# Kernel tuning notes

Measured on AMD Instinct MI355X. Metric: run time of the kernel, lower is better.

The kernel has to match this reference:

```python
import jax, jax.numpy as jnp
import numpy as np

N_NODES = 100000
N_EDGES = 600000
D_FEAT = 128
EDIM = 128
N_CLASSES = 10


def setup_inputs() -> dict:
    key = jax.random.key(0)
    k_h, k_eh, k_w, k_b, k_s, k_d = jax.random.split(key, 6)
    h = jax.random.normal(k_h, (N_NODES, D_FEAT), dtype=jnp.float32)
    edge_h = jax.random.normal(k_eh, (N_EDGES, 1, EDIM), dtype=jnp.float32)
    # Linear(in_features*2 + edim -> out_classes); torch stores weight as [out, in]
    W_w = jax.random.normal(k_w, (N_CLASSES, 2 * D_FEAT + EDIM), dtype=jnp.float32) * 0.05
    W_b = jax.random.normal(k_b, (N_CLASSES,), dtype=jnp.float32) * 0.05
    src = jax.random.randint(k_s, (N_EDGES,), 0, N_NODES, dtype=jnp.int64)
    dst = jax.random.randint(k_d, (N_EDGES,), 0, N_NODES, dtype=jnp.int64)
    return {"h": h, "edge_h": edge_h, "W_w": W_w, "W_b": W_b, "src": src, "dst": dst}


def reference(h, edge_h, W_w, W_b, src, dst):
    # edge-wise gather of src/dst node features
    h_u = h[src]                      # [E, D]
    h_v = h[dst]                      # [E, D]
    h_uv = edge_h.reshape(edge_h.shape[0], edge_h.shape[2])  # [E, edim]
    feat = jnp.concatenate([h_u, h_v, h_uv], axis=1)          # [E, 2D+edim]
    score = feat @ W_w.T + W_b                                 # [E, C]
    return score
```

## Files before the change

### kernel.cpp

```cpp
#include <hip/hip_runtime.h>


typedef __attribute__((ext_vector_type(8))) short short8;
typedef __attribute__((ext_vector_type(4))) float f32x4;

#define NC   10
#define TPW  4
#define NFRAG 12

__device__ __forceinline__ unsigned short f2bf(float f) {
    unsigned u = __builtin_bit_cast(unsigned, f);
    u += 0x7FFFu + ((u >> 16) & 1u);
    return (unsigned short)(u >> 16);
}

__device__ __forceinline__ short8 cvt8(f32x4 a, f32x4 b) {
    short8 s;
    s[0]=(short)f2bf(a[0]); s[1]=(short)f2bf(a[1]);
    s[2]=(short)f2bf(a[2]); s[3]=(short)f2bf(a[3]);
    s[4]=(short)f2bf(b[0]); s[5]=(short)f2bf(b[1]);
    s[6]=(short)f2bf(b[2]); s[7]=(short)f2bf(b[3]);
    return s;
}

__global__ void build_wfrag(const float* __restrict__ Ww, short8* __restrict__ frag) {
    const int l = threadIdx.x;
    const int n = l & 15;
    const int q = l >> 4;
#pragma unroll
    for (int t = 0; t < NFRAG; ++t) {
        short8 b = (short8)0;
        if (n < NC) {
            const float* w = Ww + n * 384 + t * 32 + q * 8;
            const f32x4 w0 = *(const f32x4*)(w);
            const f32x4 w1 = *(const f32x4*)(w + 4);
            b = cvt8(w0, w1);
        }
        frag[t * 64 + l] = b;
    }
}

#define LG(v0,v1,v2,v3,v4,v5,v6,v7,p)           \
    v0 = *(const f32x4*)((p) + 0);              \
    v1 = *(const f32x4*)((p) + 4);              \
    v2 = *(const f32x4*)((p) + 32);             \
    v3 = *(const f32x4*)((p) + 36);             \
    v4 = *(const f32x4*)((p) + 64);             \
    v5 = *(const f32x4*)((p) + 68);             \
    v6 = *(const f32x4*)((p) + 96);             \
    v7 = *(const f32x4*)((p) + 100);

#define CG(g, v0,v1,v2,v3,v4,v5,v6,v7)                                        \
    acc = __builtin_amdgcn_mfma_f32_16x16x32_bf16(cvt8(v0,v1), bf[(g)*4+0], acc, 0,0,0); \
    acc = __builtin_amdgcn_mfma_f32_16x16x32_bf16(cvt8(v2,v3), bf[(g)*4+1], acc, 0,0,0); \
    acc = __builtin_amdgcn_mfma_f32_16x16x32_bf16(cvt8(v4,v5), bf[(g)*4+2], acc, 0,0,0); \
    acc = __builtin_amdgcn_mfma_f32_16x16x32_bf16(cvt8(v6,v7), bf[(g)*4+3], acc, 0,0,0);

__global__ __launch_bounds__(64, 3) void mlp_edge_mfma(
    const float* __restrict__ h,
    const float* __restrict__ eh,
    const short8* __restrict__ frag,
    const float* __restrict__ Wb,
    const int*   __restrict__ src,
    const int*   __restrict__ dst,
    float* __restrict__ out,
    int E)
{
    const int l = threadIdx.x;
    const int n = l & 15;
    const int q = l >> 4;

    short8 bf[NFRAG];
#pragma unroll
    for (int t = 0; t < NFRAG; ++t) bf[t] = frag[t * 64 + l];
    const float bias = (n < NC) ? Wb[n] : 0.f;

    const long tile0 = (long)blockIdx.x * TPW;

#pragma unroll 1
    for (int tt = 0; tt < TPW; ++tt) {
        const long base = (tile0 + tt) * 16;
        if (base >= E) break;
        const long e  = base + n;
        const long ec = (e < E) ? e : (long)(E - 1);
        const float* ps = h  + (long)src[ec] * 128 + q * 8;
        const float* pd = h  + (long)dst[ec] * 128 + q * 8;
        const float* pe = eh + ec * 128 + q * 8;

        f32x4 x0,x1,x2,x3,x4,x5,x6,x7;
        f32x4 y0,y1,y2,y3,y4,y5,y6,y7;

        f32x4 acc = {0.f, 0.f, 0.f, 0.f};

        LG(x0,x1,x2,x3,x4,x5,x6,x7, ps)
        LG(y0,y1,y2,y3,y4,y5,y6,y7, pd)
        CG(0, x0,x1,x2,x3,x4,x5,x6,x7)
        LG(x0,x1,x2,x3,x4,x5,x6,x7, pe)
        CG(1, y0,y1,y2,y3,y4,y5,y6,y7)
        CG(2, x0,x1,x2,x3,x4,x5,x6,x7)

        if (n < NC) {
#pragma unroll
            for (int r = 0; r < 4; ++r) {
                const long e2 = base + q * 4 + r;
                if (e2 < E) out[e2 * NC + n] = acc[r] + bias;
            }
        }
    }
}

extern "C" void kernel_launch(void* const* d_in, const int* in_sizes, int n_in,
                              void* d_out, int out_size, void* d_ws, size_t ws_size,
                              hipStream_t stream) {
    const float* h   = (const float*)d_in[0];
    const float* eh  = (const float*)d_in[1];
    const float* Ww  = (const float*)d_in[2];
    const float* Wb  = (const float*)d_in[3];
    const int*   src = (const int*)d_in[4];
    const int*   dst = (const int*)d_in[5];
    float* out = (float*)d_out;

    const int E = in_sizes[4];
    short8* frag = (short8*)d_ws;

    build_wfrag<<<1, 64, 0, stream>>>(Ww, frag);

    const int edgesPerBlock = 16 * TPW;
    const int blocks = (E + edgesPerBlock - 1) / edgesPerBlock;
    mlp_edge_mfma<<<blocks, 64, 0, stream>>>(h, eh, frag, Wb, src, dst, out, E);
}
```

Before: 495.3 us.

## Stream gathered rows into LDS via async global_load_lds with triple buffering

```diff
diff --git a/kernel.cpp b/kernel.cpp
--- a/kernel.cpp
+++ b/kernel.cpp
@@ -4,9 +4,11 @@
 typedef __attribute__((ext_vector_type(8))) short short8;
 typedef __attribute__((ext_vector_type(4))) float f32x4;
 
-#define NC   10
-#define TPW  4
+#define NC    10
+#define TPW   8
 #define NFRAG 12
+
+#define WAITVM(N) __builtin_amdgcn_s_waitcnt(((N)&0xF) | (7u<<4) | (0xFu<<8) | (((unsigned)(N)>>4)<<14))
 
 __device__ __forceinline__ unsigned short f2bf(float f) {
     unsigned u = __builtin_bit_cast(unsigned, f);
@@ -23,6 +25,13 @@
     return s;
 }
 
+__device__ __forceinline__ void dma16(const void* g, void* l) {
+    __builtin_amdgcn_global_load_lds(
+        (const __attribute__((address_space(1))) void*)g,
+        (__attribute__((address_space(3))) void*)l,
+        16, 0, 0);
+}
+
 __global__ void build_wfrag(const float* __restrict__ Ww, short8* __restrict__ frag) {
     const int l = threadIdx.x;
     const int n = l & 15;
@@ -32,31 +41,13 @@
         short8 b = (short8)0;
         if (n < NC) {
             const float* w = Ww + n * 384 + t * 32 + q * 8;
-            const f32x4 w0 = *(const f32x4*)(w);
-            const f32x4 w1 = *(const f32x4*)(w + 4);
-            b = cvt8(w0, w1);
+            b = cvt8(*(const f32x4*)w, *(const f32x4*)(w + 4));
         }
         frag[t * 64 + l] = b;
     }
 }
 
-#define LG(v0,v1,v2,v3,v4,v5,v6,v7,p)           \
-    v0 = *(const f32x4*)((p) + 0);              \
-    v1 = *(const f32x4*)((p) + 4);              \
-    v2 = *(const f32x4*)((p) + 32);             \
-    v3 = *(const f32x4*)((p) + 36);             \
-    v4 = *(const f32x4*)((p) + 64);             \
-    v5 = *(const f32x4*)((p) + 68);             \
-    v6 = *(const f32x4*)((p) + 96);             \
-    v7 = *(const f32x4*)((p) + 100);
-
-#define CG(g, v0,v1,v2,v3,v4,v5,v6,v7)                                        \
-    acc = __builtin_amdgcn_mfma_f32_16x16x32_bf16(cvt8(v0,v1), bf[(g)*4+0], acc, 0,0,0); \
-    acc = __builtin_amdgcn_mfma_f32_16x16x32_bf16(cvt8(v2,v3), bf[(g)*4+1], acc, 0,0,0); \
-    acc = __builtin_amdgcn_mfma_f32_16x16x32_bf16(cvt8(v4,v5), bf[(g)*4+2], acc, 0,0,0); \
-    acc = __builtin_amdgcn_mfma_f32_16x16x32_bf16(cvt8(v6,v7), bf[(g)*4+3], acc, 0,0,0);
-
-__global__ __launch_bounds__(64, 3) void mlp_edge_mfma(
+__global__ __launch_bounds__(64, 2) void mlp_edge_dma(
     const float* __restrict__ h,
     const float* __restrict__ eh,
     const short8* __restrict__ frag,
@@ -66,44 +57,87 @@
     float* __restrict__ out,
     int E)
 {
+    __shared__ __align__(16) char buf[3][8192];
+
     const int l = threadIdx.x;
     const int n = l & 15;
     const int q = l >> 4;
+
+    const long wbase = (long)blockIdx.x * (16 * TPW);
 
     short8 bf[NFRAG];
 #pragma unroll
     for (int t = 0; t < NFRAG; ++t) bf[t] = frag[t * 64 + l];
     const float bias = (n < NC) ? Wb[n] : 0.f;
 
-    const long tile0 = (long)blockIdx.x * TPW;
+    int sidx[TPW], didx[TPW], erow[TPW];
+#pragma unroll
+    for (int t = 0; t < TPW; ++t) {
+        const long er  = wbase + t * 16 + n;
+        const long erc = (er < E) ? er : (long)(E - 1);
+        sidx[t] = src[erc];
+        didx[t] = dst[erc];
+        erow[t] = (int)erc;
+    }
 
-#pragma unroll 1
-    for (int tt = 0; tt < TPW; ++tt) {
-        const long base = (tile0 + tt) * 16;
-        if (base >= E) break;
-        const long e  = base + n;
-        const long ec = (e < E) ? e : (long)(E - 1);
-        const float* ps = h  + (long)src[ec] * 128 + q * 8;
-        const float* pd = h  + (long)dst[ec] * 128 + q * 8;
-        const float* pe = eh + ec * 128 + q * 8;
+    f32x4 acc[TPW];
+#pragma unroll
+    for (int t = 0; t < TPW; ++t) acc[t] = (f32x4){0.f, 0.f, 0.f, 0.f};
 
-        f32x4 x0,x1,x2,x3,x4,x5,x6,x7;
-        f32x4 y0,y1,y2,y3,y4,y5,y6,y7;
+    const unsigned wb16 = (unsigned)q * 16u;
 
-        f32x4 acc = {0.f, 0.f, 0.f, 0.f};
+#define ISSUE_G(t, s) do {                                                    \
+    const char* gb;                                                           \
+    unsigned off;                                                             \
+    if ((s) == 0)      { gb = (const char*)h;  off = (unsigned)sidx[t] * 512u + wb16; } \
+    else if ((s) == 1) { gb = (const char*)h;  off = (unsigned)didx[t] * 512u + wb16; } \
+    else               { gb = (const char*)eh; off = (unsigned)erow[t] * 512u + wb16; } \
+    const char* ga = gb + off;                                                \
+    char* lb = &buf[(s)][0];                                                  \
+    _Pragma("unroll")                                                         \
+    for (int i = 0; i < 8; ++i) dma16(ga + i * 64, lb + i * 1024);            \
+} while (0)
 
-        LG(x0,x1,x2,x3,x4,x5,x6,x7, ps)
-        LG(y0,y1,y2,y3,y4,y5,y6,y7, pd)
-        CG(0, x0,x1,x2,x3,x4,x5,x6,x7)
-        LG(x0,x1,x2,x3,x4,x5,x6,x7, pe)
-        CG(1, y0,y1,y2,y3,y4,y5,y6,y7)
-        CG(2, x0,x1,x2,x3,x4,x5,x6,x7)
+#define CONSUME_G(t, s) do {                                                  \
+    const char* lb = &buf[(s)][0];                                            \
+    _Pragma("unroll")                                                         \
+    for (int t4 = 0; t4 < 4; ++t4) {                                          \
+        const int ib = (2 * t4 + (q >> 1)) * 1024 + ((q & 1) * 2) * 256 + n * 16; \
+        const f32x4 a0 = *(const f32x4*)(lb + ib);                            \
+        const f32x4 a1 = *(const f32x4*)(lb + ib + 256);                      \
+        acc[t] = __builtin_amdgcn_mfma_f32_16x16x32_bf16(                     \
+            cvt8(a0, a1), bf[(s) * 4 + t4], acc[t], 0, 0, 0);                 \
+    }                                                                         \
+} while (0)
 
-        if (n < NC) {
+    WAITVM(0);
+    __asm__ volatile("" ::: "memory");
+
+    ISSUE_G(0, 0); ISSUE_G(0, 1); ISSUE_G(0, 2);
+
+#pragma unroll
+    for (int t = 0; t < TPW; ++t) {
+#pragma unroll
+        for (int s = 0; s < 3; ++s) {
+            if (t < TPW - 1 || s == 0) { WAITVM(16); }
+            else if (s == 1)           { WAITVM(8);  }
+            else                       { WAITVM(0);  }
+            __asm__ volatile("" ::: "memory");
+            CONSUME_G(t, s);
+            if (t < TPW - 1) ISSUE_G(t + 1, s);
+        }
+    }
+#undef ISSUE_G
+#undef CONSUME_G
+
+    if (n < NC) {
+#pragma unroll
+        for (int t = 0; t < TPW; ++t) {
+            const long tb = wbase + t * 16;
 #pragma unroll
             for (int r = 0; r < 4; ++r) {
-                const long e2 = base + q * 4 + r;
-                if (e2 < E) out[e2 * NC + n] = acc[r] + bias;
+                const long e2 = tb + q * 4 + r;
+                if (e2 < E) out[e2 * NC + n] = acc[t][r] + bias;
             }
         }
     }
@@ -127,5 +161,5 @@
 
     const int edgesPerBlock = 16 * TPW;
     const int blocks = (E + edgesPerBlock - 1) / edgesPerBlock;
-    mlp_edge_mfma<<<blocks, 64, 0, stream>>>(h, eh, frag, Wb, src, dst, out, E);
+    mlp_edge_dma<<<blocks, 64, 0, stream>>>(h, eh, frag, Wb, src, dst, out, E);
 }
```

Result: no change. 490.8 us (-0.9%).

## Pre-convert node features to bf16 in workspace to halve gather traffic

Applied to the files above, without the earlier changes.

```diff
diff --git a/kernel.cpp b/kernel.cpp
--- a/kernel.cpp
+++ b/kernel.cpp
@@ -4,9 +4,10 @@
 typedef __attribute__((ext_vector_type(8))) short short8;
 typedef __attribute__((ext_vector_type(4))) float f32x4;
 
-#define NC   10
-#define TPW  4
+#define NC    10
+#define TPW   4
 #define NFRAG 12
+#define FRAG_BYTES 12288
 
 __device__ __forceinline__ unsigned short f2bf(float f) {
     unsigned u = __builtin_bit_cast(unsigned, f);
@@ -32,15 +33,23 @@
         short8 b = (short8)0;
         if (n < NC) {
             const float* w = Ww + n * 384 + t * 32 + q * 8;
-            const f32x4 w0 = *(const f32x4*)(w);
-            const f32x4 w1 = *(const f32x4*)(w + 4);
-            b = cvt8(w0, w1);
+            b = cvt8(*(const f32x4*)w, *(const f32x4*)(w + 4));
         }
         frag[t * 64 + l] = b;
     }
 }
 
-#define LG(v0,v1,v2,v3,v4,v5,v6,v7,p)           \
+__global__ __launch_bounds__(256) void cvt_h_kernel(
+    const float* __restrict__ h, short8* __restrict__ hb, long n8) {
+    const long i = (long)blockIdx.x * 256 + threadIdx.x;
+    if (i < n8) {
+        const f32x4 a = *(const f32x4*)(h + i * 8);
+        const f32x4 b = *(const f32x4*)(h + i * 8 + 4);
+        hb[i] = cvt8(a, b);
+    }
+}
+
+#define LGF(v0,v1,v2,v3,v4,v5,v6,v7,p)          \
     v0 = *(const f32x4*)((p) + 0);              \
     v1 = *(const f32x4*)((p) + 4);              \
     v2 = *(const f32x4*)((p) + 32);             \
@@ -50,14 +59,10 @@
     v6 = *(const f32x4*)((p) + 96);             \
     v7 = *(const f32x4*)((p) + 100);
 
-#define CG(g, v0,v1,v2,v3,v4,v5,v6,v7)                                        \
-    acc = __builtin_amdgcn_mfma_f32_16x16x32_bf16(cvt8(v0,v1), bf[(g)*4+0], acc, 0,0,0); \
-    acc = __builtin_amdgcn_mfma_f32_16x16x32_bf16(cvt8(v2,v3), bf[(g)*4+1], acc, 0,0,0); \
-    acc = __builtin_amdgcn_mfma_f32_16x16x32_bf16(cvt8(v4,v5), bf[(g)*4+2], acc, 0,0,0); \
-    acc = __builtin_amdgcn_mfma_f32_16x16x32_bf16(cvt8(v6,v7), bf[(g)*4+3], acc, 0,0,0);
-
+template<bool BF16H>
 __global__ __launch_bounds__(64, 3) void mlp_edge_mfma(
     const float* __restrict__ h,
+    const unsigned short* __restrict__ hb,
     const float* __restrict__ eh,
     const short8* __restrict__ frag,
     const float* __restrict__ Wb,
@@ -83,21 +88,49 @@
         if (base >= E) break;
         const long e  = base + n;
         const long ec = (e < E) ? e : (long)(E - 1);
-        const float* ps = h  + (long)src[ec] * 128 + q * 8;
-        const float* pd = h  + (long)dst[ec] * 128 + q * 8;
+        const int  sA = src[ec];
+        const int  dA = dst[ec];
         const float* pe = eh + ec * 128 + q * 8;
 
-        f32x4 x0,x1,x2,x3,x4,x5,x6,x7;
-        f32x4 y0,y1,y2,y3,y4,y5,y6,y7;
+        f32x4 acc = {0.f, 0.f, 0.f, 0.f};
+        f32x4 z0,z1,z2,z3,z4,z5,z6,z7;
 
-        f32x4 acc = {0.f, 0.f, 0.f, 0.f};
-
-        LG(x0,x1,x2,x3,x4,x5,x6,x7, ps)
-        LG(y0,y1,y2,y3,y4,y5,y6,y7, pd)
-        CG(0, x0,x1,x2,x3,x4,x5,x6,x7)
-        LG(x0,x1,x2,x3,x4,x5,x6,x7, pe)
-        CG(1, y0,y1,y2,y3,y4,y5,y6,y7)
-        CG(2, x0,x1,x2,x3,x4,x5,x6,x7)
+        if constexpr (BF16H) {
+            const short8* ps = (const short8*)(hb + (size_t)sA * 128 + q * 8);
+            const short8* pd = (const short8*)(hb + (size_t)dA * 128 + q * 8);
+            short8 s0,s1,s2,s3, d0,d1,d2,d3;
+            s0 = ps[0]; s1 = ps[4]; s2 = ps[8]; s3 = ps[12];
+            d0 = pd[0]; d1 = pd[4]; d2 = pd[8]; d3 = pd[12];
+            LGF(z0,z1,z2,z3,z4,z5,z6,z7, pe)
+            acc = __builtin_amdgcn_mfma_f32_16x16x32_bf16(s0, bf[0], acc, 0,0,0);
+            acc = __builtin_amdgcn_mfma_f32_16x16x32_bf16(s1, bf[1], acc, 0,0,0);
+            acc = __builtin_amdgcn_mfma_f32_16x16x32_bf16(s2, bf[2], acc, 0,0,0);
+            acc = __builtin_amdgcn_mfma_f32_16x16x32_bf16(s3, bf[3], acc, 0,0,0);
+            acc = __builtin_amdgcn_mfma_f32_16x16x32_bf16(d0, bf[4], acc, 0,0,0);
+            acc = __builtin_amdgcn_mfma_f32_16x16x32_bf16(d1, bf[5], acc, 0,0,0);
+            acc = __builtin_amdgcn_mfma_f32_16x16x32_bf16(d2, bf[6], acc, 0,0,0);
+            acc = __builtin_amdgcn_mfma_f32_16x16x32_bf16(d3, bf[7], acc, 0,0,0);
+        } else {
+            const float* ps = h + (long)sA * 128 + q * 8;
+            const float* pd = h + (long)dA * 128 + q * 8;
+            f32x4 x0,x1,x2,x3,x4,x5,x6,x7;
+            f32x4 y0,y1,y2,y3,y4,y5,y6,y7;
+            LGF(x0,x1,x2,x3,x4,x5,x6,x7, ps)
+            LGF(y0,y1,y2,y3,y4,y5,y6,y7, pd)
+            LGF(z0,z1,z2,z3,z4,z5,z6,z7, pe)
+            acc = __builtin_amdgcn_mfma_f32_16x16x32_bf16(cvt8(x0,x1), bf[0], acc, 0,0,0);
+            acc = __builtin_amdgcn_mfma_f32_16x16x32_bf16(cvt8(x2,x3), bf[1], acc, 0,0,0);
+            acc = __builtin_amdgcn_mfma_f32_16x16x32_bf16(cvt8(x4,x5), bf[2], acc, 0,0,0);
+            acc = __builtin_amdgcn_mfma_f32_16x16x32_bf16(cvt8(x6,x7), bf[3], acc, 0,0,0);
+            acc = __builtin_amdgcn_mfma_f32_16x16x32_bf16(cvt8(y0,y1), bf[4], acc, 0,0,0);
+            acc = __builtin_amdgcn_mfma_f32_16x16x32_bf16(cvt8(y2,y3), bf[5], acc, 0,0,0);
+            acc = __builtin_amdgcn_mfma_f32_16x16x32_bf16(cvt8(y4,y5), bf[6], acc, 0,0,0);
+            acc = __builtin_amdgcn_mfma_f32_16x16x32_bf16(cvt8(y6,y7), bf[7], acc, 0,0,0);
+        }
+        acc = __builtin_amdgcn_mfma_f32_16x16x32_bf16(cvt8(z0,z1), bf[8],  acc, 0,0,0);
+        acc = __builtin_amdgcn_mfma_f32_16x16x32_bf16(cvt8(z2,z3), bf[9],  acc, 0,0,0);
+        acc = __builtin_amdgcn_mfma_f32_16x16x32_bf16(cvt8(z4,z5), bf[10], acc, 0,0,0);
+        acc = __builtin_amdgcn_mfma_f32_16x16x32_bf16(cvt8(z6,z7), bf[11], acc, 0,0,0);
 
         if (n < NC) {
 #pragma unroll
@@ -120,12 +153,22 @@
     const int*   dst = (const int*)d_in[5];
     float* out = (float*)d_out;
 
-    const int E = in_sizes[4];
+    const int E    = in_sizes[4];
+    const int N128 = in_sizes[0];
+
     short8* frag = (short8*)d_ws;
-
     build_wfrag<<<1, 64, 0, stream>>>(Ww, frag);
 
     const int edgesPerBlock = 16 * TPW;
     const int blocks = (E + edgesPerBlock - 1) / edgesPerBlock;
-    mlp_edge_mfma<<<blocks, 64, 0, stream>>>(h, eh, frag, Wb, src, dst, out, E);
+
+    const size_t need = (size_t)FRAG_BYTES + (size_t)N128 * 2;
+    if (ws_size >= need) {
+        unsigned short* hb = (unsigned short*)((char*)d_ws + FRAG_BYTES);
+        const long n8 = (long)N128 / 8;
+        cvt_h_kernel<<<(int)((n8 + 255) / 256), 256, 0, stream>>>(h, (short8*)hb, n8);
+        mlp_edge_mfma<true><<<blocks, 64, 0, stream>>>(h, hb, eh, frag, Wb, src, dst, out, E);
+    } else {
+        mlp_edge_mfma<false><<<blocks, 64, 0, stream>>>(h, nullptr, eh, frag, Wb, src, dst, out, E);
+    }
 }
```

Measured after the change: 484.9 us. 1.02x faster.
